# Optimization experiments

Hardware: AMD Instinct MI355X
Metric: run time of the kernel (lower is better)

The kernel has to match this reference:

```python
import jax, jax.numpy as jnp
import numpy as np
from jax.scipy.special import logsumexp

B, T, H, L = 64, 512, 768, 21


def setup_inputs() -> dict:
    key = jax.random.key(0)
    ks = jax.random.split(key, 8)
    hidden = jax.random.normal(ks[0], (B, T, H), jnp.float32)          # BERT last_hidden_state
    W = jax.random.normal(ks[1], (H, L), jnp.float32) * 0.02            # classifier weight
    b = jnp.zeros((L,), jnp.float32)                                    # classifier bias
    # pytorch-crf initializes all transition params uniform(-0.1, 0.1)
    start_trans = jax.random.uniform(ks[2], (L,), jnp.float32, -0.1, 0.1)
    end_trans = jax.random.uniform(ks[3], (L,), jnp.float32, -0.1, 0.1)
    transitions = jax.random.uniform(ks[4], (L, L), jnp.float32, -0.1, 0.1)
    # contiguous-prefix valid lengths; padding labeled -100 (as in HF token classification)
    lengths = jax.random.randint(ks[5], (B,), T // 2, T + 1)
    valid = jnp.arange(T)[None, :] < lengths[:, None]                   # [B,T] bool
    raw = jax.random.randint(ks[6], (B, T), 0, L)
    labels = jnp.where(valid, raw, -100).astype(jnp.int64)
    attention_mask = valid.astype(jnp.int32)
    return dict(hidden=hidden, W=W, b=b, start_trans=start_trans,
                end_trans=end_trans, transitions=transitions,
                labels=labels, attention_mask=attention_mask)


def _crf_nll(emissions, tags, mask, st, et, trans):
    """pytorch-crf forward (log-likelihood), reduction='mean', negated."""
    mf = mask.astype(emissions.dtype)                                   # [B,T]
    # --- numerator: score of the gold tag path ---
    first = tags[:, 0]
    score = st[first] + jnp.take_along_axis(emissions[:, 0], first[:, None], 1)[:, 0]
    emit = jnp.take_along_axis(emissions, tags[..., None], 2)[..., 0]   # [B,T]
    tr = trans[tags[:, :-1], tags[:, 1:]]                               # [B,T-1]
    score = score + ((tr + emit[:, 1:]) * mf[:, 1:]).sum(-1)
    last_idx = mf.sum(-1).astype(jnp.int32) - 1                         # last valid step
    last_tags = jnp.take_along_axis(tags, last_idx[:, None], 1)[:, 0]
    score = score + et[last_tags]
    # --- denominator: log partition via forward algorithm (scan over time) ---
    alpha0 = st[None, :] + emissions[:, 0]                              # [B,L]
    ems = jnp.swapaxes(emissions[:, 1:], 0, 1)                          # [T-1,B,L]
    ms = jnp.swapaxes(mask[:, 1:], 0, 1)                                # [T-1,B]

    def step(alpha, inp):
        em_t, m_t = inp
        nxt = logsumexp(alpha[:, :, None] + trans[None] + em_t[:, None, :], axis=1)
        return jnp.where(m_t[:, None], nxt, alpha), None

    alpha, _ = jax.lax.scan(step, alpha0, (ems, ms))
    logZ = logsumexp(alpha + et[None, :], axis=-1)                      # [B]
    return -jnp.mean(score - logZ)


def _viterbi(emissions, mask, st, et, trans):
    """Vectorized Viterbi decode; identity back-pointers at masked steps so the
    path stays constant past each sequence's end (matches per-sequence decode)."""
    B_, T_, L_ = emissions.shape
    score0 = st[None, :] + emissions[:, 0]                              # [B,L]
    ems = jnp.swapaxes(emissions[:, 1:], 0, 1)                          # [T-1,B,L]
    ms = jnp.swapaxes(mask[:, 1:], 0, 1)                                # [T-1,B]
    ident = jnp.arange(L_)[None, :]

    def fwd(score, inp):
        em_t, m_t = inp
        comb = score[:, :, None] + trans[None] + em_t[:, None, :]       # [B,prev,cur]
        idx = jnp.where(m_t[:, None], comb.argmax(axis=1), ident)
        score = jnp.where(m_t[:, None], comb.max(axis=1), score)
        return score, idx

    score, hist = jax.lax.scan(fwd, score0, (ems, ms))                  # hist [T-1,B,L]
    last = jnp.argmax(score + et[None, :], axis=-1)                     # [B]

    def bwd(tag, idx_t):
        prev = jnp.take_along_axis(idx_t, tag[:, None], 1)[:, 0]
        return prev, prev

    _, prevs = jax.lax.scan(bwd, last, hist, reverse=True)              # [T-1,B], forward order
    return jnp.concatenate([prevs.T, last[:, None]], axis=1)            # [B,T]


def reference(hidden, W, b, start_trans, end_trans, transitions, labels, attention_mask):
    # classifier emissions (dropout is identity in eval)
    emissions = hidden @ W + b                                          # [B,T,L]
    # CRF NLL on gold labels
    mask = (labels != -100).at[:, 0].set(True)
    tags = jnp.where(labels == -100, 0, labels).astype(jnp.int32)
    nll = _crf_nll(emissions, tags, mask, start_trans, end_trans, transitions)
    # Viterbi decode + one-hot 'logits'
    infer_mask = attention_mask.astype(bool)
    path = _viterbi(emissions, infer_mask, start_trans, end_trans, transitions)
    logits = jax.nn.one_hot(path, emissions.shape[-1], dtype=emissions.dtype)
    logits = logits * infer_mask[..., None].astype(emissions.dtype)
    return nll, logits, emissions
```

## Files before the change

### kernel.cpp

```cpp
#include <hip/hip_runtime.h>

#define Bn 64
#define Tn 512
#define Hn 768
#define Ln 21
#define EM_ELEMS (Bn*Tn*Ln)
#define NCH 16

#define DELTA_OFF 0
#define LA0_OFF   1024
#define W_OFF2    1088
#define SCORE_OFF 1152
#define TAG_OFF   1216

__device__ __forceinline__ float rl(float x, int i){
    return __int_as_float(__builtin_amdgcn_readlane(__float_as_int(x), i));
}

#define READLANES(src, A) \
    asm volatile( \
        "v_readlane_b32 %0, %[v], 0\n\t" \
        "v_readlane_b32 %1, %[v], 1\n\t" \
        "v_readlane_b32 %2, %[v], 2\n\t" \
        "v_readlane_b32 %3, %[v], 3\n\t" \
        "v_readlane_b32 %4, %[v], 4\n\t" \
        "v_readlane_b32 %5, %[v], 5\n\t" \
        "v_readlane_b32 %6, %[v], 6\n\t" \
        "v_readlane_b32 %7, %[v], 7\n\t" \
        "v_readlane_b32 %8, %[v], 8\n\t" \
        "v_readlane_b32 %9, %[v], 9\n\t" \
        "v_readlane_b32 %10, %[v], 10\n\t" \
        "v_readlane_b32 %11, %[v], 11\n\t" \
        "v_readlane_b32 %12, %[v], 12\n\t" \
        "v_readlane_b32 %13, %[v], 13\n\t" \
        "v_readlane_b32 %14, %[v], 14\n\t" \
        "v_readlane_b32 %15, %[v], 15\n\t" \
        "v_readlane_b32 %16, %[v], 16\n\t" \
        "v_readlane_b32 %17, %[v], 17\n\t" \
        "v_readlane_b32 %18, %[v], 18\n\t" \
        "v_readlane_b32 %19, %[v], 19\n\t" \
        "v_readlane_b32 %20, %[v], 20\n\t" \
        : "=s"(A[0]),"=s"(A[1]),"=s"(A[2]),"=s"(A[3]),"=s"(A[4]), \
          "=s"(A[5]),"=s"(A[6]),"=s"(A[7]),"=s"(A[8]),"=s"(A[9]), \
          "=s"(A[10]),"=s"(A[11]),"=s"(A[12]),"=s"(A[13]),"=s"(A[14]), \
          "=s"(A[15]),"=s"(A[16]),"=s"(A[17]),"=s"(A[18]),"=s"(A[19]), \
          "=s"(A[20]) \
        : [v]"v"(src))

#define VIT_STEP(WORD, S) \
    float ec = e1; e1 = e2; \
    e2 = epr[0]; epr += Ln; \
    float A[21]; \
    READLANES(sc, A); \
    float v0=A[0]+trc[0],  v1=A[1]+trc[1],  v2=A[2]+trc[2]; \
    float v3=A[3]+trc[3],  v4=A[4]+trc[4],  v5=A[5]+trc[5]; \
    float v6=A[6]+trc[6],  v7=A[7]+trc[7],  v8=A[8]+trc[8]; \
    float v9=A[9]+trc[9],  v10=A[10]+trc[10],v11=A[11]+trc[11]; \
    float v12=A[12]+trc[12],v13=A[13]+trc[13],v14=A[14]+trc[14]; \
    float v15=A[15]+trc[15],v16=A[16]+trc[16],v17=A[17]+trc[17]; \
    float v18=A[18]+trc[18],v19=A[19]+trc[19],v20=A[20]+trc[20]; \
    float a0 = fmaxf(fmaxf(v0,v1),v2); \
    float a1 = fmaxf(fmaxf(v3,v4),v5); \
    float a2 = fmaxf(fmaxf(v6,v7),v8); \
    float a3 = fmaxf(fmaxf(v9,v10),v11); \
    float a4 = fmaxf(fmaxf(v12,v13),v14); \
    float a5 = fmaxf(fmaxf(v15,v16),v17); \
    float a6 = fmaxf(fmaxf(v18,v19),v20); \
    float b0 = fmaxf(fmaxf(a0,a1),a2); \
    float b1 = fmaxf(fmaxf(a3,a4),a5); \
    float best = fmaxf(fmaxf(b0,b1),a6); \
    float scn = best + ec; \
    int mc = (int)((WORD >> (S)) & 1ull); \
    sc = mc ? scn : sc;

#define VIT_STEP_H(WORD, S, T) \
    float ec = e1; e1 = e2; \
    e2 = epr[0]; epr += Ln; \
    float A[21]; \
    READLANES(sc, A); \
    float v0=A[0]+trc[0],  v1=A[1]+trc[1],  v2=A[2]+trc[2]; \
    float v3=A[3]+trc[3],  v4=A[4]+trc[4],  v5=A[5]+trc[5]; \
    float v6=A[6]+trc[6],  v7=A[7]+trc[7],  v8=A[8]+trc[8]; \
    float v9=A[9]+trc[9],  v10=A[10]+trc[10],v11=A[11]+trc[11]; \
    float v12=A[12]+trc[12],v13=A[13]+trc[13],v14=A[14]+trc[14]; \
    float v15=A[15]+trc[15],v16=A[16]+trc[16],v17=A[17]+trc[17]; \
    float v18=A[18]+trc[18],v19=A[19]+trc[19],v20=A[20]+trc[20]; \
    float a0 = fmaxf(fmaxf(v0,v1),v2); \
    float a1 = fmaxf(fmaxf(v3,v4),v5); \
    float a2 = fmaxf(fmaxf(v6,v7),v8); \
    float a3 = fmaxf(fmaxf(v9,v10),v11); \
    float a4 = fmaxf(fmaxf(v12,v13),v14); \
    float a5 = fmaxf(fmaxf(v15,v16),v17); \
    float a6 = fmaxf(fmaxf(v18,v19),v20); \
    float b0 = fmaxf(fmaxf(a0,a1),a2); \
    float b1 = fmaxf(fmaxf(a3,a4),a5); \
    float best = fmaxf(fmaxf(b0,b1),a6); \
    float scn = best + ec; \
    int mc = (int)((WORD >> (S)) & 1ull); \
    unsigned bm = 0u; \
    bm |= (v0==best)?1u<<0:0u;  bm |= (v1==best)?1u<<1:0u;  bm |= (v2==best)?1u<<2:0u; \
    bm |= (v3==best)?1u<<3:0u;  bm |= (v4==best)?1u<<4:0u;  bm |= (v5==best)?1u<<5:0u; \
    bm |= (v6==best)?1u<<6:0u;  bm |= (v7==best)?1u<<7:0u;  bm |= (v8==best)?1u<<8:0u; \
    bm |= (v9==best)?1u<<9:0u;  bm |= (v10==best)?1u<<10:0u; bm |= (v11==best)?1u<<11:0u; \
    bm |= (v12==best)?1u<<12:0u; bm |= (v13==best)?1u<<13:0u; bm |= (v14==best)?1u<<14:0u; \
    bm |= (v15==best)?1u<<15:0u; bm |= (v16==best)?1u<<16:0u; bm |= (v17==best)?1u<<17:0u; \
    bm |= (v18==best)?1u<<18:0u; bm |= (v19==best)?1u<<19:0u; bm |= (v20==best)?1u<<20:0u; \
    int bpv = __ffs(bm) - 1; \
    int bps = mc ? bpv : j; \
    if (act) hg[(size_t)(T)*Ln + j] = (unsigned char)bps; \
    sc = mc ? scn : sc;

#define NLL_STEP(WORD, S) \
    float ec = e1; e1 = e2; \
    e2 = epr[0]; epr += Ln; \
    float pe = __expf(ec); \
    float A[21]; \
    READLANES(p, A); \
    float s0=0.f,s1=0.f,s2=0.f; \
    _Pragma("unroll") \
    for (int i=0;i<Ln;++i){ \
        if      (i%3==0) s0 = fmaf(A[i], Ec[i], s0); \
        else if (i%3==1) s1 = fmaf(A[i], Ec[i], s1); \
        else             s2 = fmaf(A[i], Ec[i], s2); \
    } \
    float pn = ((s0+s1)+s2) * pe; \
    int lc = (int)((WORD >> (S)) & 1ull); \
    p = lc ? pn : p; \
    if (((S) & 7) == 0){ \
        float p0 = rl(p, 0); \
        int e; frexpf(p0, &e); \
        p = ldexpf(p, -e); \
        M += (float)e * 0.6931471805599453f; \
    }

__global__ __launch_bounds__(256) void emis_kernel(
    const float* __restrict__ hidden, const float* __restrict__ W,
    const float* __restrict__ bias, float* __restrict__ em)
{
    __shared__ float part[4][64][22];
    const int lane = threadIdx.x & 63;
    const int w    = threadIdx.x >> 6;
    const int row  = blockIdx.x*64 + lane;
    const int cl   = (lane < 21) ? lane : 20;
    const float4* h4 = (const float4*)(hidden + (size_t)row*Hn) + w*48;
    const float*  Wc = W + (size_t)(w*192)*Ln;
    float acc[Ln];
    #pragma unroll
    for (int j=0;j<Ln;++j) acc[j]=0.f;
    for (int tb=0; tb<12; ++tb){
        float4 hb[4];
        float Wk[16];
        #pragma unroll
        for (int q=0;q<4;++q) hb[q] = h4[tb*4+q];
        #pragma unroll
        for (int kk=0;kk<16;++kk) Wk[kk] = Wc[(size_t)(tb*16+kk)*Ln + cl];
        #pragma unroll
        for (int q=0;q<4;++q){
            const float* hv = &hb[q].x;
            #pragma unroll
            for (int c=0;c<4;++c){
                float x = hv[c];
                float A[21];
                READLANES(Wk[q*4+c], A);
                #pragma unroll
                for (int j=0;j<Ln;++j)
                    acc[j] = fmaf(x, A[j], acc[j]);
            }
        }
    }
    #pragma unroll
    for (int j=0;j<Ln;++j) part[w][lane][j] = acc[j];
    __syncthreads();
    float* ob = em + (size_t)blockIdx.x*64*Ln;
    for (int e=threadIdx.x; e<64*Ln; e+=256){
        int r = e/Ln, j = e-r*Ln;
        ob[e] = ((part[0][r][j]+part[1][r][j])+(part[2][r][j]+part[3][r][j])) + bias[j];
    }
}

__global__ __launch_bounds__(64) void chunk_scan(
    const float* __restrict__ em, const int* __restrict__ labels,
    const int* __restrict__ amask, const float* __restrict__ st,
    const float* __restrict__ et, const float* __restrict__ trans,
    float* __restrict__ ws, float* __restrict__ logits)
{
    __shared__ float em_s[66*Ln];

    const int mode = blockIdx.x >> 10;
    const int idx  = blockIdx.x & 1023;
    const int b    = idx >> 4;
    const int c    = idx & (NCH-1);
    const int lane = threadIdx.x;
    const bool act = (lane < Ln);
    const int  j   = act ? lane : 0;

    const int tstart = c*32;
    const int WARM   = (c==0) ? 0 : 32;
    const int w0     = tstart - WARM;
    const int nrows  = WARM + 32;

    const float* emg = em + (size_t)b*Tn*Ln;
    for (int i=lane; i<nrows*Ln; i+=64) em_s[i] = emg[(size_t)w0*Ln + i];
    for (int i=lane; i<2*Ln; i+=64){
        int jj = (i < Ln) ? i : (i - Ln);
        em_s[nrows*Ln + i] = em_s[(nrows-1)*Ln + jj];
    }
    __syncthreads();

    if (mode == 0){
        const int* mk = amask + b*Tn;
        int last = -1;
        #pragma unroll
        for (int k=0;k<8;++k){ int mv = mk[k*64+lane]; if (mv) last = k*64+lane; }
        #pragma unroll
        for (int off=32; off>=1; off>>=1){ int o = __shfl_xor(last, off, 64); last = (o>last)?o:last; }
        const bool owner = (last >= tstart) && (last < tstart+32);

        unsigned long long word = __ballot(mk[w0 + lane] != 0);

        float trc[Ln];
        #pragma unroll
        for (int i=0;i<Ln;++i) trc[i] = trans[i*Ln + j];

        float sc;
        if (c==0) sc = act ? (st[j] + em_s[j]) : -1e30f;
        else      sc = act ? 0.f : -1e30f;

        unsigned char* hg = (unsigned char*)(logits + (size_t)b*Tn*Ln);

        const float* epr = &em_s[Ln + j];
        float e1 = epr[0]; epr += Ln;
        float e2 = epr[0]; epr += Ln;

        if (c > 0){
            for (int s=1; s<32; ++s){
                VIT_STEP(word, s)
            }
        }
        const int s0i = (c==0) ? 1 : 0;
        for (int s=s0i; s<32; ++s){
            VIT_STEP_H(word, WARM + s, tstart + s)
        }
        if (owner){
            float val = act ? (sc + et[j]) : -1e30f;
            int   tix = act ? j : 1000;
            #pragma unroll
            for (int off=32; off>=1; off>>=1){
                float ov = __shfl_xor(val, off, 64);
                int   oi = __shfl_xor(tix, off, 64);
                if (ov > val || (ov==val && oi<tix)){ val=ov; tix=oi; }
            }
            if (lane==0) ((int*)(ws+TAG_OFF))[b] = tix;
        }
    } else {
        const int* lb = labels + b*Tn;
        int last = -1;
        #pragma unroll
        for (int k=0;k<8;++k){ int mv = (lb[k*64+lane] != -100) ? 1 : 0; if (mv) last = k*64+lane; }
        #pragma unroll
        for (int off=32; off>=1; off>>=1){ int o = __shfl_xor(last, off, 64); last = (o>last)?o:last; }
        const bool owner = (last >= tstart) && (last < tstart+32);

        unsigned long long word = __ballot(lb[w0 + lane] != -100);

        float Ec[Ln];
        #pragma unroll
        for (int i=0;i<Ln;++i) Ec[i] = __expf(trans[i*Ln + j]);

        float p, M = 0.f, La;
        if (c==0){
            p = act ? __expf(st[j] + em_s[j]) : 0.f;
            float sm = p;
            #pragma unroll
            for (int off=32; off>=1; off>>=1) sm += __shfl_xor(sm, off, 64);
            La = __logf(sm);
        } else {
            p = act ? 1.f : 0.f;
            La = 0.f;
        }

        const float* epr = &em_s[Ln + j];
        float e1 = epr[0]; epr += Ln;
        float e2 = epr[0]; epr += Ln;

        if (c > 0){
            for (int s=1; s<32; ++s){
                NLL_STEP(word, s)
            }
            float sm = act ? p : 0.f;
            #pragma unroll
            for (int off=32; off>=1; off>>=1) sm += __shfl_xor(sm, off, 64);
            La = M + __logf(sm);
        }
        const int s0i = (c==0) ? 1 : 0;
        for (int s=s0i; s<32; ++s){
            NLL_STEP(word, WARM + s)
        }
        float sm = act ? p : 0.f;
        #pragma unroll
        for (int off=32; off>=1; off>>=1) sm += __shfl_xor(sm, off, 64);
        float Lb = M + __logf(sm);
        if (lane==0) (ws+DELTA_OFF)[b*NCH + c] = Lb - La;
        if (c==0 && lane==0) (ws+LA0_OFF)[b] = La;
        if (owner){
            float wsum = act ? (p * __expf(et[j])) : 0.f;
            #pragma unroll
            for (int off=32; off>=1; off>>=1) wsum += __shfl_xor(wsum, off, 64);
            if (lane==0) (ws+W_OFF2)[b] = __logf(wsum) - __logf(sm);
        }
    }
}

__global__ __launch_bounds__(512) void post_kernel(
    const float* __restrict__ em, const int* __restrict__ labels,
    const int* __restrict__ amask, const float* __restrict__ st,
    const float* __restrict__ et, const float* __restrict__ trans,
    float* __restrict__ ws, float* __restrict__ logits)
{
    const int b    = blockIdx.x & (Bn-1);
    const int mode = blockIdx.x >> 6;
    const int tid  = threadIdx.x;

    if (mode == 0){
        __shared__ unsigned char hist_s[Tn*Ln];
        __shared__ int lab_s[Tn];
        __shared__ int path_s[Tn];
        __shared__ unsigned char comp_s[64*Ln];
        __shared__ unsigned char ent_s[64];
        lab_s[tid] = amask[b*Tn + tid];
        const unsigned char* hg = (const unsigned char*)(logits + (size_t)b*Tn*Ln);
        for (int i=tid; i<Tn*Ln; i+=512) hist_s[i] = hg[i];
        __syncthreads();
        if (tid < 64){
            unsigned char cur[Ln];
            #pragma unroll
            for (int q=0;q<Ln;++q) cur[q] = (unsigned char)q;
            #pragma unroll
            for (int k=8;k>=1;--k){
                int ta = 8*tid + k;
                if (ta < Tn){
                    const unsigned char* hr = &hist_s[ta*Ln];
                    #pragma unroll
                    for (int q=0;q<Ln;++q) cur[q] = hr[cur[q]];
                }
            }
            #pragma unroll
            for (int q=0;q<Ln;++q) comp_s[tid*Ln+q] = cur[q];
        }
        __syncthreads();
        if (tid==0){
            int cg = ((const int*)(ws+TAG_OFF))[b];
            for (int l=63;l>=0;--l){ ent_s[l]=(unsigned char)cg; cg = comp_s[l*Ln+cg]; }
        }
        __syncthreads();
        if (tid < 64){
            int s = ent_s[tid];
            if (tid==63) path_s[Tn-1] = s;
            #pragma unroll
            for (int k=8;k>=1;--k){
                int ta = 8*tid + k;
                if (ta < Tn){ s = hist_s[ta*Ln+s]; path_s[ta-1] = s; }
            }
        }
        __syncthreads();
        float* lg = logits + (size_t)b*Tn*Ln;
        for (int id2=tid; id2<Tn*Ln; id2+=512){
            int t = id2/Ln; int jj = id2 - t*Ln;
            lg[id2] = (lab_s[t] && path_s[t]==jj) ? 1.0f : 0.0f;
        }
    } else {
        __shared__ float red_s[8];
        __shared__ int  redc_s[8];
        const int* lb = labels + b*Tn;
        int labt = lb[tid];
        float term = 0.f;
        int c = (tid==0 || labt != -100) ? 1 : 0;
        if (tid>=1 && labt != -100){
            int lp = lb[tid-1]; if (lp<0) lp=0;
            term = trans[lp*Ln+labt] + em[((size_t)b*Tn+tid)*Ln + labt];
        }
        #pragma unroll
        for (int off=32; off>=1; off>>=1){
            term += __shfl_xor(term, off, 64);
            c    += __shfl_xor(c,    off, 64);
        }
        int w = tid>>6;
        if ((tid&63)==0){ red_s[w]=term; redc_s[w]=c; }
        __syncthreads();
        if (tid==0){
            float sum=0.f; int cnt=0;
            #pragma unroll
            for (int q=0;q<8;++q){ sum+=red_s[q]; cnt+=redc_s[q]; }
            int l0 = lb[0]; int tag0 = l0<0?0:l0;
            float score = st[tag0] + em[(size_t)b*Tn*Ln + tag0] + sum;
            int li = cnt-1; int ll = lb[li]; int lt = ll<0?0:ll;
            score += et[lt];
            (ws+SCORE_OFF)[b] = score;
        }
    }
}

__global__ __launch_bounds__(64) void fin_kernel(const float* __restrict__ ws,
                                                 float* __restrict__ out0)
{
    const int b = threadIdx.x;
    float logZ = (ws+LA0_OFF)[b] + (ws+W_OFF2)[b];
    #pragma unroll
    for (int c=0;c<NCH;++c) logZ += (ws+DELTA_OFF)[b*NCH + c];
    float v = (ws+SCORE_OFF)[b] - logZ;
    #pragma unroll
    for (int off=32; off>=1; off>>=1) v += __shfl_xor(v, off, 64);
    if (b==0) out0[0] = -(v * (1.0f/64.0f));
}

extern "C" void kernel_launch(void* const* d_in, const int* in_sizes, int n_in,
                              void* d_out, int out_size, void* d_ws, size_t ws_size,
                              hipStream_t stream)
{
    (void)in_sizes; (void)n_in; (void)out_size; (void)ws_size;
    const float* hidden = (const float*)d_in[0];
    const float* W      = (const float*)d_in[1];
    const float* bias   = (const float*)d_in[2];
    const float* st     = (const float*)d_in[3];
    const float* et     = (const float*)d_in[4];
    const float* trans  = (const float*)d_in[5];
    const int*   labels = (const int*)d_in[6];
    const int*   amask  = (const int*)d_in[7];

    float* out    = (float*)d_out;
    float* nll    = out;
    float* logits = out + 1;
    float* em     = out + 1 + EM_ELEMS;
    float* ws     = (float*)d_ws;

    emis_kernel<<<dim3(Bn*Tn/64), dim3(256), 0, stream>>>(hidden, W, bias, em);
    chunk_scan<<<dim3(2048), dim3(64), 0, stream>>>(em, labels, amask, st, et, trans, ws, logits);
    post_kernel<<<dim3(2*Bn), dim3(512), 0, stream>>>(em, labels, amask, st, et, trans, ws, logits);
    fin_kernel<<<dim3(1), dim3(64), 0, stream>>>(ws, nll);
}
```

Measured before the change: 64.91 us.

## Stage hidden rows and weight slices through shared memory in emission GEMM

The emission kernel now loads each 64-row by 192-column hidden tile into padded shared memory with coalesced cooperative loads, plus the matching W slice, in four phases. Each wave then reads its k-slice from LDS instead of each lane streaming its own row with strided float4 loads. This is meant to improve global-memory coalescing for the 100 MB hidden read. In exchange it adds per-phase barriers, scalar (non-vector) global loads, and about 64 KB of LDS per block, which lowers occupancy and leaves no overlap between loading and compute.

```diff
diff --git a/kernel.cpp b/kernel.cpp
--- a/kernel.cpp
+++ b/kernel.cpp
@@ -137,44 +137,57 @@
     const float* __restrict__ hidden, const float* __restrict__ W,
     const float* __restrict__ bias, float* __restrict__ em)
 {
-    __shared__ float part[4][64][22];
-    const int lane = threadIdx.x & 63;
-    const int w    = threadIdx.x >> 6;
-    const int row  = blockIdx.x*64 + lane;
+    __shared__ float smem[16384];
+    float* hs = smem;
+    float* Wl = smem + 12352;
+    const int tid  = threadIdx.x;
+    const int lane = tid & 63;
+    const int w    = tid >> 6;
+    const int blk  = blockIdx.x;
     const int cl   = (lane < 21) ? lane : 20;
-    const float4* h4 = (const float4*)(hidden + (size_t)row*Hn) + w*48;
-    const float*  Wc = W + (size_t)(w*192)*Ln;
     float acc[Ln];
     #pragma unroll
     for (int j=0;j<Ln;++j) acc[j]=0.f;
-    for (int tb=0; tb<12; ++tb){
-        float4 hb[4];
-        float Wk[16];
-        #pragma unroll
-        for (int q=0;q<4;++q) hb[q] = h4[tb*4+q];
-        #pragma unroll
-        for (int kk=0;kk<16;++kk) Wk[kk] = Wc[(size_t)(tb*16+kk)*Ln + cl];
-        #pragma unroll
-        for (int q=0;q<4;++q){
-            const float* hv = &hb[q].x;
-            #pragma unroll
-            for (int c=0;c<4;++c){
-                float x = hv[c];
+
+    for (int p=0;p<4;++p){
+        __syncthreads();
+        for (int i=tid; i<64*192; i+=256){
+            int r = i/192, kk = i - r*192;
+            hs[r*193+kk] = hidden[(size_t)(blk*64+r)*Hn + p*192 + kk];
+        }
+        for (int i=tid; i<192*Ln; i+=256)
+            Wl[i] = W[(size_t)p*192*Ln + i];
+        __syncthreads();
+        const int kb = 48*w;
+        for (int tb=0; tb<3; ++tb){
+            float xk[16], Wk[16];
+            #pragma unroll
+            for (int q=0;q<16;++q){
+                int kl = kb + tb*16 + q;
+                xk[q] = hs[lane*193 + kl];
+                Wk[q] = Wl[kl*Ln + cl];
+            }
+            #pragma unroll
+            for (int q=0;q<16;++q){
                 float A[21];
-                READLANES(Wk[q*4+c], A);
+                READLANES(Wk[q], A);
+                float x = xk[q];
                 #pragma unroll
                 for (int j=0;j<Ln;++j)
                     acc[j] = fmaf(x, A[j], acc[j]);
             }
         }
     }
+    __syncthreads();
+    float* part = smem;
     #pragma unroll
-    for (int j=0;j<Ln;++j) part[w][lane][j] = acc[j];
+    for (int j=0;j<Ln;++j) part[(w*64 + lane)*22 + j] = acc[j];
     __syncthreads();
-    float* ob = em + (size_t)blockIdx.x*64*Ln;
-    for (int e=threadIdx.x; e<64*Ln; e+=256){
+    float* ob = em + (size_t)blk*64*Ln;
+    for (int e=tid; e<64*Ln; e+=256){
         int r = e/Ln, j = e-r*Ln;
-        ob[e] = ((part[0][r][j]+part[1][r][j])+(part[2][r][j]+part[3][r][j])) + bias[j];
+        ob[e] = ((part[(0*64+r)*22+j]+part[(1*64+r)*22+j])
+               +(part[(2*64+r)*22+j]+part[(3*64+r)*22+j])) + bias[j];
     }
 }
 
```

Result: slower. 98.70 us (+52.1%).
